# Kernel optimization log

Measured on AMD Instinct MI355X. Metric: run time of the kernel, lower is better.

## Reference

```python
import jax, jax.numpy as jnp
import numpy as np

GROUP = 64
DIM = 4096
N_HEADS = 32
N_KV = 8
HEAD_DIM = DIM // N_HEADS  # 128
N_REP = N_HEADS // N_KV    # 4
B = 1
S = 2048
THETA = 1e6


def _pack_q40(rng, out_f, in_f):
    """Random int4 weights packed Q4_0 style (two nibbles per int8) + per-group scales."""
    q = rng.integers(-7, 8, size=(out_f * in_f,)).reshape(-1, 2, GROUP)
    packed = ((q[:, 0] << 4) | (q[:, 1] & 15)).astype(np.int8)  # [out*in/group/2, group]
    scale = (np.abs(rng.standard_normal((out_f * in_f // GROUP, 1))) * 0.01 + 1e-3).astype(np.float32)
    return jnp.asarray(packed), jnp.asarray(scale)


def dequantize_q40(w, scale, shape):
    """Faithful port of torch dequantize_q40: arithmetic shifts sign-extend nibbles."""
    msb = jnp.right_shift(w, 4)                          # high nibble, sign-extended
    lsb = jnp.right_shift(jnp.left_shift(w, 4), 4)       # low nibble, sign-extended
    grp = jnp.concatenate([msb, lsb], axis=1).reshape(-1, GROUP)  # hstack then view(-1, group)
    return (grp.astype(scale.dtype) * scale).reshape(shape)


def setup_inputs() -> dict:
    rng = np.random.default_rng(0)
    wq, sq = _pack_q40(rng, N_HEADS * HEAD_DIM, DIM)
    wk, sk = _pack_q40(rng, N_KV * HEAD_DIM, DIM)
    wv, sv = _pack_q40(rng, N_KV * HEAD_DIM, DIM)
    wo, so = _pack_q40(rng, DIM, N_HEADS * HEAD_DIM)
    x = jnp.asarray(rng.standard_normal((B, S, DIM)), jnp.float32)
    inv_freq = 1.0 / (THETA ** (np.arange(0, HEAD_DIM, 2, dtype=np.float64) / HEAD_DIM))
    ang = np.outer(np.arange(S, dtype=np.float64), inv_freq)  # [S, HEAD_DIM/2]
    cos = jnp.asarray(np.cos(ang), jnp.float32)
    sin = jnp.asarray(np.sin(ang), jnp.float32)
    causal = np.triu(np.ones((S, S), dtype=bool), k=1)
    mask = jnp.asarray(np.where(causal, -1e9, 0.0), jnp.float32)
    return dict(x=x, wq=wq, sq=sq, wk=wk, sk=sk, wv=wv, sv=sv, wo=wo, so=so,
                cos=cos, sin=sin, mask=mask)


def _rotate_half(t):
    h = t.shape[-1] // 2
    return jnp.concatenate([-t[..., h:], t[..., :h]], axis=-1)


def reference(x, wq, sq, wk, sk, wv, sv, wo, so, cos, sin, mask):
    # Dequant-then-matmul QKV projections (weights stored as [out, in])
    Wq = dequantize_q40(wq, sq, (N_HEADS * HEAD_DIM, DIM))
    Wk = dequantize_q40(wk, sk, (N_KV * HEAD_DIM, DIM))
    Wv = dequantize_q40(wv, sv, (N_KV * HEAD_DIM, DIM))
    Wo = dequantize_q40(wo, so, (DIM, N_HEADS * HEAD_DIM))

    xq = (x @ Wq.T).reshape(B, S, N_HEADS, HEAD_DIM)
    xk = (x @ Wk.T).reshape(B, S, N_KV, HEAD_DIM)
    xv = (x @ Wv.T).reshape(B, S, N_KV, HEAD_DIM)

    # RoPE (rotate-half convention): cos/sin are [S, HEAD_DIM/2] -> cat to [S, HEAD_DIM]
    cosf = jnp.concatenate([cos, cos], axis=-1)[:, None, :]  # [S, 1, HEAD_DIM]
    sinf = jnp.concatenate([sin, sin], axis=-1)[:, None, :]
    xq = xq * cosf + _rotate_half(xq) * sinf
    xk = xk * cosf + _rotate_half(xk) * sinf

    # start_pos == 0 prefill: keys/values are the freshly projected xk/xv
    # GQA: repeat_interleave over the kv-head dim
    keys = jnp.repeat(xk, N_REP, axis=2)    # [B, S, N_HEADS, HEAD_DIM]
    values = jnp.repeat(xv, N_REP, axis=2)

    scores = jnp.einsum('bqhd,bkhd->bhqk', xq, keys) / np.float32(np.sqrt(HEAD_DIM))
    scores = scores + mask  # additive causal mask broadcast over [B, H]
    attn = jax.nn.softmax(scores, axis=-1)
    out = jnp.einsum('bhqk,bkhd->bqhd', attn, values).reshape(B, S, N_HEADS * HEAD_DIM)
    return out @ Wo.T
```

## Files before the change

kernel.cpp:

```cpp
#include <hip/hip_runtime.h>
#include <stdint.h>

#define DIMX 4096
#define NH   32
#define NKV  8
#define HD   128
#define SEQ  2048
#define QKVD 6144

typedef _Float16 h16;
typedef __attribute__((ext_vector_type(8))) _Float16 h16x8;
typedef __attribute__((ext_vector_type(4))) _Float16 h16x4;
typedef __attribute__((ext_vector_type(4))) float   f32x4;

__device__ __forceinline__ void gload_lds16(const void* g, void* l) {
  __builtin_amdgcn_global_load_lds(
      (const __attribute__((address_space(1))) void*)g,
      (__attribute__((address_space(3))) void*)l, 16, 0, 0);
}

template <int CTRL>
__device__ __forceinline__ float dpp_mv(float x) {
  int y = __builtin_amdgcn_mov_dpp(__builtin_bit_cast(int, x), CTRL, 0xF, 0xF, true);
  return __builtin_bit_cast(float, y);
}
__device__ __forceinline__ float red16_max(float x) {
  x = fmaxf(x, dpp_mv<0xB1>(x));
  x = fmaxf(x, dpp_mv<0x1B>(x));
  x = fmaxf(x, dpp_mv<0x141>(x));
  x = fmaxf(x, dpp_mv<0x140>(x));
  return x;
}
__device__ __forceinline__ float red16_sum(float x) {
  x += dpp_mv<0xB1>(x);
  x += dpp_mv<0x1B>(x);
  x += dpp_mv<0x141>(x);
  x += dpp_mv<0x140>(x);
  return x;
}

template <int PERM>
__device__ __forceinline__ void dq_unit(const void* __restrict__ w, const float* __restrict__ sc,
                                        h16* __restrict__ out, int u, int flag) {
  uint32_t b4;
  if (flag) {
    const int4 t = *(const int4*)((const int*)w + 4 * u);
    b4 = (uint32_t)(t.x & 0xFF) | ((uint32_t)(t.y & 0xFF) << 8) |
         ((uint32_t)(t.z & 0xFF) << 16) | ((uint32_t)(t.w & 0xFF) << 24);
  } else {
    b4 = ((const uint32_t*)w)[u];
  }
  int r = u >> 4;
  int p = (u & 15) * 4;
  float shi = sc[2 * r], slo = sc[2 * r + 1];
  h16x4 hi, lo;
#pragma unroll
  for (int j = 0; j < 4; ++j) {
    int by = (int)((b4 >> (8 * j)) & 0xFF);
    int hn = (by << 24) >> 28;
    int ln = (by << 28) >> 28;
    hi[j] = (h16)((float)hn * shi);
    lo[j] = (h16)((float)ln * slo);
  }
  size_t base;
  if (PERM) {
    int row  = r >> 5;
    int rowp = (row & ~127) | (((row & 63) << 1) | ((row >> 6) & 1));
    base = ((size_t)rowp << 12) + (size_t)((r & 31) << 7);
  } else {
    base = (size_t)r << 7;
  }
  *(h16x4*)(out + base + p)      = hi;
  *(h16x4*)(out + base + 64 + p) = lo;
}

#define U_WQ 2097152
#define U_WK 524288
#define U_WV 524288
#define U_WO 2097152

__global__ __launch_bounds__(256) void prep_all(
    const void* __restrict__ wq, const float* __restrict__ sq,
    const void* __restrict__ wk, const float* __restrict__ sk,
    const void* __restrict__ wv, const float* __restrict__ sv,
    const void* __restrict__ wo, const float* __restrict__ so,
    const float4* __restrict__ x,
    h16* __restrict__ Wqkv, h16* __restrict__ Wo, h16x4* __restrict__ xb) {
  __shared__ int sfl;
  if (threadIdx.x == 0) {
    int ok = 1;
    const int* wi = (const int*)wq;
    for (int i = 0; i < 64; ++i) {
      int v = wi[i];
      if (v < -128 || v > 127) ok = 0;
    }
    sfl = ok;
  }
  __syncthreads();
  const int fl = sfl;
  int u = blockIdx.x * 256 + threadIdx.x;
  if (u < U_WQ) { dq_unit<1>(wq, sq, Wqkv, u, fl); return; }
  u -= U_WQ;
  if (u < U_WK) { dq_unit<1>(wk, sk, Wqkv + 16777216, u, fl); return; }
  u -= U_WK;
  if (u < U_WV) { dq_unit<0>(wv, sv, Wqkv + 20971520, u, fl); return; }
  u -= U_WV;
  if (u < U_WO) { dq_unit<0>(wo, so, Wo, u, fl); return; }
  u -= U_WO;
  {
    float4 v = x[u];
    h16x4 o;
    o.x = (h16)v.x; o.y = (h16)v.y; o.z = (h16)v.z; o.w = (h16)v.w;
    xb[u] = o;
  }
}

template <typename OutT, int NT, int MODE>
__global__ __launch_bounds__(512, 2) void gemm_pipe(
    const h16* __restrict__ A, const h16* __restrict__ B, OutT* __restrict__ C,
    int N, int K,
    const float* __restrict__ cosb, const float* __restrict__ sinb,
    h16* __restrict__ vt) {
  constexpr int NSLOT = 4 + NT;
  constexpr int BUFH  = NSLOT * 4096;
  __shared__ __attribute__((aligned(16))) h16 SM[2 * BUFH];

  const int tid  = threadIdx.x;
  const int w    = tid >> 6, lane = tid & 63;
  const int wr   = w >> 1, wc = w & 1;
  const int quad = lane >> 4, l15 = lane & 15;
  const int axr  = l15 & 7;
  const int m0 = blockIdx.y * 256, n0 = blockIdx.x * (NT * 64);

  const h16* Ab = A + (size_t)m0 * K;
  const h16* Bb = B + (size_t)n0 * K;
  const int srow = tid >> 3;
  const int sg8  = ((tid & 7) ^ (srow & 7)) * 8;

  f32x4 acc[2][2][2][NT];
#pragma unroll
  for (int a = 0; a < 2; ++a)
#pragma unroll
    for (int b = 0; b < 2; ++b)
#pragma unroll
      for (int mt = 0; mt < 2; ++mt)
#pragma unroll
        for (int nt = 0; nt < NT; ++nt) acc[a][b][mt][nt] = (f32x4){0.f, 0.f, 0.f, 0.f};

  h16x8 af[2][2][2];
  h16x8 bf1[NT][2];
  h16x8 bf0E[NT][2], bf0O[NT][2];

#define STG(sl_, tile_) do {                                                        \
    const h16* g_ = ((sl_) < 4) ? (Ab + (size_t)((sl_) * 64) * K)                   \
                                : (Bb + (size_t)(((sl_) - 4) * 64) * K);            \
    char* d_ = (char*)(SM + ((tile_) & 1) * BUFH + (sl_) * 4096);                   \
    gload_lds16(g_ + (size_t)srow * K + (tile_) * 64 + sg8, d_ + tid * 16);         \
  } while (0)

#define LDA_(tile_, a_) do {                                                        \
    const h16* s_ = SM + ((tile_) & 1) * BUFH + wr * 4096;                          \
    _Pragma("unroll") for (int mt = 0; mt < 2; ++mt)                                \
    _Pragma("unroll") for (int ks = 0; ks < 2; ++ks)                                \
      af[a_][mt][ks] = *(const h16x8*)&s_[((a_) * 32 + mt * 16 + l15) * 64 +        \
                                          (((ks * 4 + quad) ^ axr) * 8)];           \
  } while (0)

#define LDB1_(tile_) do {                                                           \
    const h16* s_ = SM + ((tile_) & 1) * BUFH + 16384;                              \
    _Pragma("unroll") for (int nt = 0; nt < NT; ++nt)                               \
    _Pragma("unroll") for (int ks = 0; ks < 2; ++ks)                                \
      bf1[nt][ks] = *(const h16x8*)&s_[(NT * 32 + wc * (NT * 16) + nt * 16 + l15) * 64 + \
                                       (((ks * 4 + quad) ^ axr) * 8)];              \
  } while (0)

#define LDB0_(tile_, D_) do {                                                       \
    const h16* s_ = SM + ((tile_) & 1) * BUFH + 16384;                              \
    _Pragma("unroll") for (int nt = 0; nt < NT; ++nt)                               \
    _Pragma("unroll") for (int ks = 0; ks < 2; ++ks)                                \
      D_[nt][ks] = *(const h16x8*)&s_[(wc * (NT * 16) + nt * 16 + l15) * 64 +       \
                                      (((ks * 4 + quad) ^ axr) * 8)];               \
  } while (0)

#define MMAB1(a_) do {                                                              \
    __builtin_amdgcn_s_setprio(1);                                                  \
    _Pragma("unroll") for (int mt = 0; mt < 2; ++mt)                                \
    _Pragma("unroll") for (int nt = 0; nt < NT; ++nt)                               \
    _Pragma("unroll") for (int ks = 0; ks < 2; ++ks)                                \
      acc[a_][1][mt][nt] = __builtin_amdgcn_mfma_f32_16x16x32_f16(                  \
          af[a_][mt][ks], bf1[nt][ks], acc[a_][1][mt][nt], 0, 0, 0);                \
    __builtin_amdgcn_s_setprio(0);                                                  \
  } while (0)

#define MMAB0(a_, D_) do {                                                          \
    __builtin_amdgcn_s_setprio(1);                                                  \
    _Pragma("unroll") for (int mt = 0; mt < 2; ++mt)                                \
    _Pragma("unroll") for (int nt = 0; nt < NT; ++nt)                               \
    _Pragma("unroll") for (int ks = 0; ks < 2; ++ks)                                \
      acc[a_][0][mt][nt] = __builtin_amdgcn_mfma_f32_16x16x32_f16(                  \
          af[a_][mt][ks], D_[nt][ks], acc[a_][0][mt][nt], 0, 0, 0);                 \
    __builtin_amdgcn_s_setprio(0);                                                  \
  } while (0)

#define CFENCE asm volatile("" ::: "memory")
#define BARX do { CFENCE; __builtin_amdgcn_s_barrier(); CFENCE; } while (0)
#define VM5  asm volatile("s_waitcnt vmcnt(5)" ::: "memory")
#define VM2  asm volatile("s_waitcnt vmcnt(2)" ::: "memory")
#define VMP4 do { if constexpr (NT == 3) asm volatile("s_waitcnt vmcnt(2)" ::: "memory"); \
                  else                   asm volatile("s_waitcnt vmcnt(1)" ::: "memory"); } while (0)
#define VM0  asm volatile("s_waitcnt vmcnt(0)" ::: "memory")

  const int NTILE = K >> 6;
  const int NIT   = K >> 7;

  if constexpr (NT == 3) {
    STG(4, 0); STG(5, 0); STG(0, 0); STG(1, 0); STG(2, 0); STG(3, 0); STG(6, 0);
    STG(4, 1); STG(5, 1);
    VMP4;
  } else {
    STG(4, 0); STG(0, 0); STG(1, 0); STG(2, 0); STG(3, 0); STG(5, 0);
    STG(4, 1);
    VMP4;
  }
  BARX;
  LDA_(0, 0); LDB0_(0, bf0E);

  for (int i = 0; i < NIT; ++i) {
    const int t0 = 2 * i, t1 = 2 * i + 1;
    const int T2 = (t0 + 2 < NTILE) ? t0 + 2 : NTILE - 1;
    const int T3 = (t1 + 2 < NTILE) ? t1 + 2 : NTILE - 1;
    LDB1_(t0);
    STG(0, t1); STG(1, t1); STG(2, t1); STG(3, t1);
    MMAB0(0, bf0E); BARX;
    LDA_(t0, 1);
    if constexpr (NT == 3) STG(6, t1); else STG(5, t1);
    VM5;
    MMAB1(0); BARX;
    LDB0_(t1, bf0O);
    STG(4, T2);
    VM2;
    MMAB1(1); BARX;
    LDA_(t1, 0);
    if constexpr (NT == 3) STG(5, T2);
    VMP4;
    MMAB0(1, bf0E); BARX;
    LDB1_(t1);
    STG(0, T2); STG(1, T2); STG(2, T2); STG(3, T2);
    MMAB0(0, bf0O); BARX;
    LDA_(t1, 1);
    if constexpr (NT == 3) STG(6, T2); else STG(5, T2);
    VM5;
    MMAB1(0); BARX;
    LDB0_(T2, bf0E);
    STG(4, T3);
    VM2;
    MMAB1(1); BARX;
    LDA_(T2, 0);
    if constexpr (NT == 3) STG(5, T3);
    VMP4;
    MMAB0(1, bf0O); BARX;
  }
  VM0;

  if constexpr (MODE == 1) {
#pragma unroll
    for (int a = 0; a < 2; ++a)
#pragma unroll
      for (int b = 0; b < 2; ++b)
#pragma unroll
        for (int mt = 0; mt < 2; ++mt)
#pragma unroll
          for (int nt = 0; nt < NT; ++nt) {
            const int cb   = n0 + b * (NT * 32) + wc * (NT * 16) + nt * 16;
            const int row0 = m0 + wr * 64 + a * 32 + mt * 16 + quad * 4;
            if (cb >= 5120) {
              const int dcol = cb + l15 - 5120;
              h16x4 vvv;
#pragma unroll
              for (int r = 0; r < 4; ++r) vvv[r] = (h16)acc[a][b][mt][nt][r];
              *(h16x4*)(vt + (size_t)dcol * SEQ + row0) = vvv;
            } else {
              const int col = cb + l15;
              const int j   = (col & 127) >> 1;
              const float sgn = (col & 1) ? 1.f : -1.f;
#pragma unroll
              for (int r = 0; r < 4; ++r) {
                float own = acc[a][b][mt][nt][r];
                float par = dpp_mv<0xB1>(own);
                float cc  = cosb[(size_t)(row0 + r) * 64 + j];
                float ss  = sinb[(size_t)(row0 + r) * 64 + j];
                C[(size_t)(row0 + r) * N + col] = (OutT)(own * cc + sgn * par * ss);
              }
            }
          }
  } else {
#pragma unroll
    for (int a = 0; a < 2; ++a)
#pragma unroll
      for (int b = 0; b < 2; ++b)
#pragma unroll
        for (int mt = 0; mt < 2; ++mt)
#pragma unroll
          for (int nt = 0; nt < NT; ++nt)
#pragma unroll
            for (int r = 0; r < 4; ++r) {
              int row = m0 + wr * 64 + a * 32 + mt * 16 + quad * 4 + r;
              int col = n0 + b * (NT * 32) + wc * (NT * 16) + nt * 16 + l15;
              C[(size_t)row * N + col] = (OutT)acc[a][b][mt][nt][r];
            }
  }
#undef STG
#undef LDA_
#undef LDB1_
#undef LDB0_
#undef MMAB1
#undef MMAB0
#undef CFENCE
#undef BARX
#undef VM5
#undef VM2
#undef VMP4
#undef VM0
}

__global__ __launch_bounds__(256, 2) void flash_attn(
    const h16* __restrict__ qkv, const h16* __restrict__ vt, h16* __restrict__ o_out) {
  __shared__ __attribute__((aligned(16))) h16 Ks[64 * 128];
  __shared__ __attribute__((aligned(16))) h16 Vts[128 * 64];
  __shared__ __attribute__((aligned(16))) h16 Ps[4][32 * 72];

  const int tid  = threadIdx.x;
  const int w    = tid >> 6, lane = tid & 63;
  const int quad = lane >> 4, l15 = lane & 15;
  const int h    = blockIdx.x;
  const int y    = blockIdx.y;
  const int qt   = (y < 8) ? (15 - y) : (y - 8);
  const int kv   = h >> 2;
  const int rowq = qt * 128 + w * 32;
  const h16* vtg = vt + (size_t)kv * HD * SEQ;

  h16x8 qf[2][4];
#pragma unroll
  for (int mt = 0; mt < 2; ++mt) {
    const h16* qrow = qkv + (size_t)(rowq + mt * 16 + l15) * QKVD + h * 128;
#pragma unroll
    for (int ks = 0; ks < 4; ++ks)
      qf[mt][ks] = *(const h16x8*)(qrow + ks * 32 + quad * 8);
  }

  f32x4 o[2][8];
#pragma unroll
  for (int mt = 0; mt < 2; ++mt)
#pragma unroll
    for (int i = 0; i < 8; ++i) o[mt][i] = (f32x4){0.f, 0.f, 0.f, 0.f};
  float mrow[2][4], lrow[2][4];
#pragma unroll
  for (int mt = 0; mt < 2; ++mt)
#pragma unroll
    for (int r = 0; r < 4; ++r) { mrow[mt][r] = -3e30f; lrow[mt][r] = 0.f; }
  h16* Psw = Ps[w];

  const int nkt = 2 * qt + 2;
  for (int kt = 0; kt < nkt; ++kt) {
    const int k0 = kt * 64;
    __syncthreads();
#pragma unroll
    for (int i = 0; i < 4; ++i) {
      int c = i * 256 + tid;
      int key = c >> 4, d8s = c & 15;
      gload_lds16(qkv + (size_t)(k0 + key) * QKVD + 4096 + kv * 128 + (d8s ^ (key & 15)) * 8,
                  (char*)Ks + c * 16);
    }
#pragma unroll
    for (int i = 0; i < 4; ++i) {
      int c = i * 256 + tid;
      int d = c >> 3, p = c & 7;
      gload_lds16(vtg + (size_t)d * SEQ + k0 + (p ^ (d & 7)) * 8,
                  (char*)Vts + c * 16);
    }
    __syncthreads();

    if (k0 <= rowq + 31) {
      const float sscale = 0.08838834764831845f;
      float alpha[2][4];
      f32x4 s2[2][4];
#pragma unroll
      for (int nt = 0; nt < 4; ++nt) {
        int key = nt * 16 + l15;
        f32x4 a0 = (f32x4){0.f, 0.f, 0.f, 0.f};
        f32x4 a1 = (f32x4){0.f, 0.f, 0.f, 0.f};
#pragma unroll
        for (int ks = 0; ks < 4; ++ks) {
          int d8 = ks * 4 + quad;
          h16x8 kf = *(const h16x8*)&Ks[key * 128 + ((d8 ^ (key & 15)) * 8)];
          a0 = __builtin_amdgcn_mfma_f32_16x16x32_f16(qf[0][ks], kf, a0, 0, 0, 0);
          a1 = __builtin_amdgcn_mfma_f32_16x16x32_f16(qf[1][ks], kf, a1, 0, 0, 0);
        }
        s2[0][nt] = a0;
        s2[1][nt] = a1;
      }
#pragma unroll
      for (int mt = 0; mt < 2; ++mt) {
#pragma unroll
        for (int r = 0; r < 4; ++r) {
          int rowg = rowq + mt * 16 + quad * 4 + r;
          float pv[4];
          float tm = -3e30f;
#pragma unroll
          for (int nt = 0; nt < 4; ++nt) {
            float v = s2[mt][nt][r] * sscale;
            if (k0 + nt * 16 + l15 > rowg) v = -3e30f;
            pv[nt] = v;
            tm = fmaxf(tm, v);
          }
          tm = red16_max(tm);
          float mnew = fmaxf(mrow[mt][r], tm);
          float a = __expf(mrow[mt][r] - mnew);
          mrow[mt][r] = mnew;
          alpha[mt][r] = a;
          float ps = 0.f;
#pragma unroll
          for (int nt = 0; nt < 4; ++nt) {
            float e = __expf(pv[nt] - mnew);
            ps += e;
            Psw[(mt * 16 + quad * 4 + r) * 72 + nt * 16 + l15] = (h16)e;
          }
          ps = red16_sum(ps);
          lrow[mt][r] = lrow[mt][r] * a + ps;
        }
      }
#pragma unroll
      for (int mt = 0; mt < 2; ++mt)
#pragma unroll
        for (int on = 0; on < 8; ++on) {
          o[mt][on][0] *= alpha[mt][0]; o[mt][on][1] *= alpha[mt][1];
          o[mt][on][2] *= alpha[mt][2]; o[mt][on][3] *= alpha[mt][3];
        }
      asm volatile("s_waitcnt lgkmcnt(0)" ::: "memory");
#pragma unroll
      for (int ks = 0; ks < 2; ++ks) {
        h16x8 pf0 = *(const h16x8*)&Psw[(0  + l15) * 72 + ks * 32 + quad * 8];
        h16x8 pf1 = *(const h16x8*)&Psw[(16 + l15) * 72 + ks * 32 + quad * 8];
        int k8 = ks * 4 + quad;
#pragma unroll
        for (int on = 0; on < 8; ++on) {
          int d = on * 16 + l15;
          h16x8 vf = *(const h16x8*)&Vts[d * 64 + ((k8 ^ (d & 7)) * 8)];
          o[0][on] = __builtin_amdgcn_mfma_f32_16x16x32_f16(pf0, vf, o[0][on], 0, 0, 0);
          o[1][on] = __builtin_amdgcn_mfma_f32_16x16x32_f16(pf1, vf, o[1][on], 0, 0, 0);
        }
      }
    }
  }
#pragma unroll
  for (int mt = 0; mt < 2; ++mt) {
    float linv[4];
#pragma unroll
    for (int r = 0; r < 4; ++r) linv[r] = 1.0f / lrow[mt][r];
#pragma unroll
    for (int on = 0; on < 8; ++on)
#pragma unroll
      for (int r = 0; r < 4; ++r) {
        int row = rowq + mt * 16 + quad * 4 + r;
        int col = h * 128 + on * 16 + l15;
        o_out[(size_t)row * DIMX + col] = (h16)(o[mt][on][r] * linv[r]);
      }
  }
}

extern "C" void kernel_launch(void* const* d_in, const int* in_sizes, int n_in,
                              void* d_out, int out_size, void* d_ws, size_t ws_size,
                              hipStream_t stream) {
  const float* x    = (const float*)d_in[0];
  const void*  wq   = d_in[1];
  const float* sq   = (const float*)d_in[2];
  const void*  wk   = d_in[3];
  const float* sk   = (const float*)d_in[4];
  const void*  wv   = d_in[5];
  const float* sv   = (const float*)d_in[6];
  const void*  wo   = d_in[7];
  const float* so   = (const float*)d_in[8];
  const float* cosb = (const float*)d_in[9];
  const float* sinb = (const float*)d_in[10];
  float* out = (float*)d_out;

  char* ws = (char*)d_ws;
  h16* Wqkv = (h16*)ws;
  h16* Wo   = (h16*)(ws + 50331648);
  h16* xb   = (h16*)(ws + 83886080);
  h16* qkv  = (h16*)(ws + 100663296);
  h16* vt   = (h16*)d_out;

  prep_all<<<28672, 256, 0, stream>>>(wq, sq, wk, sk, wv, sv, wo, so,
                                      (const float4*)x, Wqkv, Wo, (h16x4*)xb);

  gemm_pipe<h16, 3, 1><<<dim3(32, 8), 512, 0, stream>>>(
      xb, Wqkv, qkv, QKVD, DIMX, cosb, sinb, vt);

  flash_attn<<<dim3(32, 16), 256, 0, stream>>>(qkv, vt, xb);

  gemm_pipe<float, 2, 0><<<dim3(32, 8), 512, 0, stream>>>(
      xb, Wo, out, DIMX, DIMX, cosb, sinb, vt);
}
```

Baseline: 433.4 us.

## Deepen GEMM prefetch by staging two full k-tiles ahead with relaxed waitcnts

Reorders the global-to-LDS staging in the GEMM main loop so both tiles t0 and t1 are fully issued in the prologue, and each iteration prefetches tile T2/T3 further ahead. The vmcnt waits are loosened (up to 7 outstanding loads) so more global loads stay in flight while MFMAs run, hiding memory latency. This relies on the LDS buffer slot reuse staying race-free under the new ordering and could add LDS pressure or hazards if the waits are off.

Result: no change. 426.1 us (-1.7%).

```diff
diff --git a/kernel.cpp b/kernel.cpp
--- a/kernel.cpp
+++ b/kernel.cpp
@@ -204,24 +204,22 @@
 
 #define CFENCE asm volatile("" ::: "memory")
 #define BARX do { CFENCE; __builtin_amdgcn_s_barrier(); CFENCE; } while (0)
-#define VM5  asm volatile("s_waitcnt vmcnt(5)" ::: "memory")
-#define VM2  asm volatile("s_waitcnt vmcnt(2)" ::: "memory")
-#define VMP4 do { if constexpr (NT == 3) asm volatile("s_waitcnt vmcnt(2)" ::: "memory"); \
-                  else                   asm volatile("s_waitcnt vmcnt(1)" ::: "memory"); } while (0)
+#define W2 do { if constexpr (NT == 3) asm volatile("s_waitcnt vmcnt(7)" ::: "memory"); \
+                else                   asm volatile("s_waitcnt vmcnt(6)" ::: "memory"); } while (0)
+#define W3 do { if constexpr (NT == 3) asm volatile("s_waitcnt vmcnt(3)" ::: "memory"); \
+                else                   asm volatile("s_waitcnt vmcnt(2)" ::: "memory"); } while (0)
 #define VM0  asm volatile("s_waitcnt vmcnt(0)" ::: "memory")
 
   const int NTILE = K >> 6;
   const int NIT   = K >> 7;
 
-  if constexpr (NT == 3) {
-    STG(4, 0); STG(5, 0); STG(0, 0); STG(1, 0); STG(2, 0); STG(3, 0); STG(6, 0);
-    STG(4, 1); STG(5, 1);
-    VMP4;
-  } else {
-    STG(4, 0); STG(0, 0); STG(1, 0); STG(2, 0); STG(3, 0); STG(5, 0);
-    STG(4, 1);
-    VMP4;
-  }
+  STG(4, 0); STG(5, 0);
+  if constexpr (NT == 3) STG(6, 0);
+  STG(0, 0); STG(1, 0); STG(2, 0); STG(3, 0);
+  STG(4, 1); STG(5, 1);
+  if constexpr (NT == 3) STG(6, 1);
+  STG(0, 1); STG(1, 1); STG(2, 1); STG(3, 1);
+  W2;
   BARX;
   LDA_(0, 0); LDB0_(0, bf0E);
 
@@ -230,34 +228,24 @@
     const int T2 = (t0 + 2 < NTILE) ? t0 + 2 : NTILE - 1;
     const int T3 = (t1 + 2 < NTILE) ? t1 + 2 : NTILE - 1;
     LDB1_(t0);
-    STG(0, t1); STG(1, t1); STG(2, t1); STG(3, t1);
     MMAB0(0, bf0E); BARX;
-    LDA_(t0, 1);
-    if constexpr (NT == 3) STG(6, t1); else STG(5, t1);
-    VM5;
+    LDA_(t0, 1); STG(4, T2); W2;
     MMAB1(0); BARX;
-    LDB0_(t1, bf0O);
-    STG(4, T2);
-    VM2;
+    LDB0_(t1, bf0O); STG(5, T2);
+    if constexpr (NT == 3) STG(6, T2);
+    W3;
     MMAB1(1); BARX;
-    LDA_(t1, 0);
-    if constexpr (NT == 3) STG(5, T2);
-    VMP4;
+    LDA_(t1, 0); STG(0, T2); STG(1, T2); STG(2, T2); STG(3, T2);
     MMAB0(1, bf0E); BARX;
     LDB1_(t1);
-    STG(0, T2); STG(1, T2); STG(2, T2); STG(3, T2);
     MMAB0(0, bf0O); BARX;
-    LDA_(t1, 1);
-    if constexpr (NT == 3) STG(6, T2); else STG(5, T2);
-    VM5;
+    LDA_(t1, 1); STG(4, T3); W2;
     MMAB1(0); BARX;
-    LDB0_(T2, bf0E);
-    STG(4, T3);
-    VM2;
+    LDB0_(T2, bf0E); STG(5, T3);
+    if constexpr (NT == 3) STG(6, T3);
+    W3;
     MMAB1(1); BARX;
-    LDA_(T2, 0);
-    if constexpr (NT == 3) STG(5, T3);
-    VMP4;
+    LDA_(T2, 0); STG(0, T3); STG(1, T3); STG(2, T3); STG(3, T3);
     MMAB0(1, bf0O); BARX;
   }
   VM0;
@@ -317,9 +305,8 @@
 #undef MMAB0
 #undef CFENCE
 #undef BARX
-#undef VM5
-#undef VM2
-#undef VMP4
+#undef W2
+#undef W3
 #undef VM0
 }
 
```
